# Optimization experiments

Measured on AMD Instinct MI355X. Metric: run time of the kernel, lower is better.

The kernel has to match this reference:

```python
import jax, jax.numpy as jnp
import numpy as np
from jax import lax

B, N, D, H = 8, 2048, 512, 1024


def setup_inputs() -> dict:
    key = jax.random.key(0)
    k0, k1, k2 = jax.random.split(key, 3)
    x = jax.random.normal(k0, (B, N, D), jnp.float32)
    conv_w = jax.random.normal(k1, (H, D, 3), jnp.float32) * (1.0 / np.sqrt(3 * D))
    conv_b = jnp.zeros((H,), jnp.float32)
    ln_g = jnp.ones((H,), jnp.float32)
    ln_b = jnp.zeros((H,), jnp.float32)
    proj_w = jax.random.normal(k2, (H, 2), jnp.float32) * (1.0 / np.sqrt(H))
    proj_b = jnp.zeros((2,), jnp.float32)
    return dict(x=x, conv_w=conv_w, conv_b=conv_b, ln_g=ln_g, ln_b=ln_b,
                proj_w=proj_w, proj_b=proj_b)


def reference(x, conv_w, conv_b, ln_g, ln_b, proj_w, proj_b):
    b, n, _ = x.shape
    # Conv1d(input_dim->hidden, k=3, pad=1) on [B, C, N]
    h = lax.conv_general_dilated(x.transpose(0, 2, 1), conv_w, (1,), [(1, 1)],
                                 dimension_numbers=('NCH', 'OIH', 'NCH'))
    h = h.transpose(0, 2, 1) + conv_b          # [B, N, H]
    h = jax.nn.relu(h)
    # LayerNorm over hidden dim (dropout is identity at inference)
    mu = jnp.mean(h, axis=-1, keepdims=True)
    var = jnp.mean((h - mu) ** 2, axis=-1, keepdims=True)
    h = (h - mu) * lax.rsqrt(var + 1e-5) * ln_g + ln_b
    groups_probs = h @ proj_w + proj_b          # [B, N, 2]

    g = jnp.argmax(groups_probs, axis=-1)       # [B, N] in {0,1}
    pos = jnp.arange(n)
    base = (pos + 1).astype(jnp.float32)        # 1..N
    # col 0 forced 0; start positions (g==1, pos>0) forced 0
    zero_mask = (pos[None, :] == 0) | ((g == 1) & (pos[None, :] > 0))
    vals = jnp.where(zero_mask, 0.0, jnp.broadcast_to(base[None, :], (b, n)))
    vals = vals.at[:, -1].set(float(n))         # last col = N (overrides zeroing)
    # stable descending sort by nonzero-ness == stable ascending sort by (val==0)
    order = jnp.argsort((vals == 0.0).astype(jnp.int32), axis=1)
    groups = jnp.take_along_axis(vals, order, axis=1)[:, :, None]  # [B, N, 1]

    t = base[None, None, :]                     # [1, 1, N], values 1..N
    # row 0: 1[t <= groups[:,0]]
    row0 = jnp.clip(groups[:, 0, :][:, None, :] - t + 1.0, 0.0, 1.0)      # [B, 1, N]
    # rows 1..: 1[groups[:,i-1] < t <= groups[:,i]]
    rest = (jnp.clip(groups[:, 1:, :] - t + 1.0, 0.0, 1.0)
            * jnp.clip(t - groups[:, :-1, :], 0.0, 1.0))                   # [B, N-1, N]
    grouping_matrix = jnp.concatenate([row0, rest], axis=1)                # [B, N, N]
    return (groups_probs, grouping_matrix)
```

## Files before the change

### kernel.cpp

```cpp
#include <hip/hip_runtime.h>

#define Bsz 8
#define Nsz 2048
#define Dsz 512
#define Hsz 1024
#define K3D 1536

typedef __attribute__((ext_vector_type(8))) short short8;
typedef __attribute__((ext_vector_type(4))) float f32x4;

static __device__ __forceinline__ unsigned short f2bf(float f) {
    unsigned u = __builtin_bit_cast(unsigned, f);
    unsigned r = (u + 0x7FFFu + ((u >> 16) & 1u)) >> 16;
    return (unsigned short)r;
}
static __device__ __forceinline__ float bf2f(unsigned short u) {
    return __builtin_bit_cast(float, (unsigned)u << 16);
}
static __device__ __forceinline__ void gld16(const void* g, void* l) {
    __builtin_amdgcn_global_load_lds(
        (const __attribute__((address_space(1))) void*)g,
        (__attribute__((address_space(3))) void*)l, 16, 0, 0);
}


__global__ __launch_bounds__(256) void prep_kernel(
    const float* __restrict__ cw, unsigned short* __restrict__ wsh,
    unsigned short* __restrict__ wsl,
    const float* __restrict__ lng, const float* __restrict__ lnb,
    const float* __restrict__ pw, float* __restrict__ CD,
    float* __restrict__ gq0, float* __restrict__ gq1)
{
    __shared__ float red[4][4];
    int blk = blockIdx.x, tid = threadIdx.x;
    if (blk < 192) {
        int gid = blk * 256 + tid;
        int s = gid >> 10, h = gid & 1023;
        int t = s >> 4, c = s & 15;
        const float* src = cw + (size_t)h * K3D + (size_t)c * 96 + t;
        short hv[32], lv[32];
        #pragma unroll
        for (int j = 0; j < 32; ++j) {
            float v = src[3 * j];
            unsigned short hi = f2bf(v);
            hv[j] = (short)hi;
            lv[j] = (short)f2bf(v - bf2f(hi));
        }
        #pragma unroll
        for (int m = 0; m < 4; ++m) {
            size_t dst = (((size_t)s * 4 + m) * 1024 + h) * 16;
            *(short8*)((char*)wsh + dst) = *(short8*)&hv[m * 8];
            *(short8*)((char*)wsl + dst) = *(short8*)&lv[m * 8];
        }
    } else if (blk == 192) {
        float c0 = 0.f, c1 = 0.f, d0 = 0.f, d1 = 0.f;
        for (int h = tid; h < Hsz; h += 256) {
            float g = lng[h], b = lnb[h];
            float w0 = pw[2 * h], w1 = pw[2 * h + 1];
            c0 = fmaf(g, w0, c0); c1 = fmaf(g, w1, c1);
            d0 = fmaf(b, w0, d0); d1 = fmaf(b, w1, d1);
        }
        #pragma unroll
        for (int m = 32; m >= 1; m >>= 1) {
            c0 += __shfl_xor(c0, m, 64); c1 += __shfl_xor(c1, m, 64);
            d0 += __shfl_xor(d0, m, 64); d1 += __shfl_xor(d1, m, 64);
        }
        int w = tid >> 6;
        if ((tid & 63) == 0) { red[w][0] = c0; red[w][1] = c1; red[w][2] = d0; red[w][3] = d1; }
        __syncthreads();
        if (tid == 0) {
            CD[0] = red[0][0] + red[1][0] + red[2][0] + red[3][0];
            CD[1] = red[0][1] + red[1][1] + red[2][1] + red[3][1];
            CD[2] = red[0][2] + red[1][2] + red[2][2] + red[3][2];
            CD[3] = red[0][3] + red[1][3] + red[2][3] + red[3][3];
        }
    } else {
        int h = (blk - 193) * 256 + tid;
        float g = lng[h];
        gq0[h] = g * pw[2 * h];
        gq1[h] = g * pw[2 * h + 1];
    }
}

__global__ __launch_bounds__(256) void convert_x_kernel(
    const float* __restrict__ x, unsigned short* __restrict__ xsh,
    unsigned short* __restrict__ xsl)
{
    int tid = threadIdx.x;
    int r = blockIdx.x * 4 + (tid >> 6);
    int e = tid & 63;
    int b  = r / 2050;
    int rp = r - b * 2050;
    int c  = e >> 2;
    int qq = e & 3;
    size_t dst = ((((size_t)b * 16 + c) * 4 + qq) * 2050 + rp) * 16;
    short8 hv, lv;
    if (rp == 0 || rp == 2049) {
        #pragma unroll
        for (int u = 0; u < 8; ++u) { hv[u] = 0; lv[u] = 0; }
    } else {
        const float* p = x + ((size_t)b * Nsz + (rp - 1)) * Dsz + e * 8;
        float4 v0 = *(const float4*)p;
        float4 v1 = *(const float4*)(p + 4);
        float vv[8] = { v0.x, v0.y, v0.z, v0.w, v1.x, v1.y, v1.z, v1.w };
        #pragma unroll
        for (int u = 0; u < 8; ++u) {
            unsigned short h = f2bf(vv[u]);
            hv[u] = (short)h;
            lv[u] = (short)f2bf(vv[u] - bf2f(h));
        }
    }
    *(short8*)((char*)xsh + dst) = hv;
    *(short8*)((char*)xsl + dst) = lv;
}

__global__ __launch_bounds__(512, 2) void gemm7_kernel(
    const unsigned short* __restrict__ xsh, const unsigned short* __restrict__ xsl,
    const unsigned short* __restrict__ wsh, const unsigned short* __restrict__ wsl,
    const float* __restrict__ cb, const float* __restrict__ gq0,
    const float* __restrict__ gq1, float* __restrict__ part)
{
    __shared__ __align__(16) char lds[131072];

    int tid = threadIdx.x;
    int swz = (blockIdx.x & 7) * 32 + (blockIdx.x >> 3);
    int mt  = swz >> 2;
    int ntb = swz & 3;
    int bb  = mt >> 3;
    int n0  = (mt & 7) * 256;
    int n0c = ntb * 256;
    int n0g = bb * Nsz + (mt & 7) * 256;

    int l = tid & 63, w = tid >> 6;
    int wr = w >> 2, wc = w & 3;
    int r = l & 15, qq = l >> 4;
    int aoff_r = qq * 4096 + (wr * 128 + r) * 16;
    int boff_r = qq * 4096 + (wc * 64 + r) * 16;

    const char* pAh = (const char*)xsh + (size_t)bb * 2099200 + (w & 3) * 32800 + (size_t)(n0 + l) * 16;
    const char* pAl = (const char*)xsl + (size_t)bb * 2099200 + (w & 3) * 32800 + (size_t)(n0 + l) * 16;
    const char* pBh = (const char*)wsh + (w & 3) * 16384 + (size_t)(n0c + l) * 16;
    const char* pBl = (const char*)wsl + (w & 3) * 16384 + (size_t)(n0c + l) * 16;

    f32x4 acc[8][4];
    #pragma unroll
    for (int i = 0; i < 8; ++i)
        #pragma unroll
        for (int j = 0; j < 4; ++j) acc[i][j] = (f32x4){0.f, 0.f, 0.f, 0.f};

#define STAGE(lb, sn) do {                                                     \
    if (w < 4) {                                                               \
        size_t ao = (size_t)(((sn) & 15) * 131200 + ((sn) >> 4) * 16);         \
        _Pragma("unroll") for (int g = 0; g < 4; ++g) {                        \
            gld16(pAh + ao + g * 1024, (lb) +         w * 4096 + g * 1024);    \
            gld16(pAl + ao + g * 1024, (lb) + 16384 + w * 4096 + g * 1024);    \
        }                                                                      \
    } else {                                                                   \
        size_t bo = (size_t)(sn) * 65536;                                      \
        _Pragma("unroll") for (int g = 0; g < 4; ++g) {                        \
            gld16(pBh + bo + g * 1024, (lb) + 32768 + (w - 4) * 4096 + g * 1024); \
            gld16(pBl + bo + g * 1024, (lb) + 49152 + (w - 4) * 4096 + g * 1024); \
        }                                                                      \
    }                                                                          \
} while (0)

    STAGE(lds, 0);

    for (int s = 0; s < 48; ++s) {
        char* cur = lds + (s & 1) * 65536;
        if (s < 47) {
            STAGE(lds + ((s + 1) & 1) * 65536, s + 1);
            asm volatile("s_waitcnt vmcnt(8)" ::: "memory");
        } else {
            asm volatile("s_waitcnt vmcnt(0)" ::: "memory");
        }
        __builtin_amdgcn_s_barrier();
        asm volatile("" ::: "memory");

        short8 bh[4], bl[4];
        #pragma unroll
        for (int j = 0; j < 4; ++j) {
            bh[j] = *(const short8*)(cur + 32768 + boff_r + j * 256);
            bl[j] = *(const short8*)(cur + 49152 + boff_r + j * 256);
        }
        #pragma unroll
        for (int mh = 0; mh < 2; ++mh) {
            short8 ah[4], al[4];
            #pragma unroll
            for (int i = 0; i < 4; ++i) {
                ah[i] = *(const short8*)(cur +         aoff_r + (mh * 4 + i) * 256);
                al[i] = *(const short8*)(cur + 16384 + aoff_r + (mh * 4 + i) * 256);
            }
            __builtin_amdgcn_s_setprio(1);
            #pragma unroll
            for (int i = 0; i < 4; ++i)
                #pragma unroll
                for (int j = 0; j < 4; ++j) {
                    acc[mh*4+i][j] = __builtin_amdgcn_mfma_f32_16x16x32_bf16(ah[i], bh[j], acc[mh*4+i][j], 0, 0, 0);
                    acc[mh*4+i][j] = __builtin_amdgcn_mfma_f32_16x16x32_bf16(ah[i], bl[j], acc[mh*4+i][j], 0, 0, 0);
                    acc[mh*4+i][j] = __builtin_amdgcn_mfma_f32_16x16x32_bf16(al[i], bh[j], acc[mh*4+i][j], 0, 0, 0);
                }
            __builtin_amdgcn_s_setprio(0);
        }
        __builtin_amdgcn_s_barrier();
    }
#undef STAGE

    float cbv[4], g0v[4], g1v[4];
    #pragma unroll
    for (int j = 0; j < 4; ++j) {
        int col = n0c + wc * 64 + j * 16 + r;
        cbv[j] = cb[col]; g0v[j] = gq0[col]; g1v[j] = gq1[col];
    }
    int slot = ntb * 16 + wc * 4;
    #pragma unroll
    for (int m = 0; m < 8; ++m) {
        #pragma unroll
        for (int reg = 0; reg < 4; ++reg) {
            float v0 = 0.f, v2 = 0.f, va = 0.f, vb = 0.f;
            #pragma unroll
            for (int j = 0; j < 4; ++j) {
                float v = acc[m][j][reg] + cbv[j];
                v = fmaxf(v, 0.f);
                v0 += v;
                v2 = fmaf(v, v, v2);
                va = fmaf(v, g0v[j], va);
                vb = fmaf(v, g1v[j], vb);
            }
            #pragma unroll
            for (int msk = 1; msk < 16; msk <<= 1) {
                v0 += __shfl_xor(v0, msk, 64); v2 += __shfl_xor(v2, msk, 64);
                va += __shfl_xor(va, msk, 64); vb += __shfl_xor(vb, msk, 64);
            }
            if (r == 0) {
                int rowg = n0g + wr * 128 + m * 16 + qq * 4 + reg;
                *(f32x4*)(part + (size_t)rowg * 64 + slot) = (f32x4){v0, v2, va, vb};
            }
        }
    }
}

__global__ __launch_bounds__(256) void probs_kernel(
    const float* __restrict__ part, const float* __restrict__ CD,
    const float* __restrict__ pb, float* __restrict__ probs,
    int* __restrict__ gout)
{
    int row = blockIdx.x * 256 + threadIdx.x;
    float S0 = 0.f, S2 = 0.f, Sa = 0.f, Sb = 0.f;
    const float4* p = (const float4*)(part + (size_t)row * 64);
    #pragma unroll
    for (int c = 0; c < 16; ++c) {
        float4 v = p[c];
        S0 += v.x; S2 += v.y; Sa += v.z; Sb += v.w;
    }
    float mu  = S0 * (1.0f / Hsz);
    float var = S2 * (1.0f / Hsz) - mu * mu;
    float rsq = 1.0f / sqrtf(var + 1e-5f);
    float p0 = fmaf(rsq, Sa - mu * CD[0], CD[2] + pb[0]);
    float p1 = fmaf(rsq, Sb - mu * CD[1], CD[3] + pb[1]);
    probs[(size_t)row * 2]     = p0;
    probs[(size_t)row * 2 + 1] = p1;
    gout[row] = (p1 > p0) ? 1 : 0;
}

#define ROWS 64
#define CCH 128
#define NCC (Hsz / CCH)
#define DSTEP 32

__global__ __launch_bounds__(256) void consts_kernel(
    const float* __restrict__ lng, const float* __restrict__ lnb,
    const float* __restrict__ pw, float* __restrict__ CD)
{
    int tid = threadIdx.x;
    float c0 = 0.f, c1 = 0.f, d0 = 0.f, d1 = 0.f;
    for (int h = tid; h < Hsz; h += 256) {
        float g = lng[h], b = lnb[h];
        float w0 = pw[2 * h], w1 = pw[2 * h + 1];
        c0 = fmaf(g, w0, c0); c1 = fmaf(g, w1, c1);
        d0 = fmaf(b, w0, d0); d1 = fmaf(b, w1, d1);
    }
    #pragma unroll
    for (int m = 32; m >= 1; m >>= 1) {
        c0 += __shfl_xor(c0, m, 64); c1 += __shfl_xor(c1, m, 64);
        d0 += __shfl_xor(d0, m, 64); d1 += __shfl_xor(d1, m, 64);
    }
    __shared__ float red[4][4];
    int w = tid >> 6;
    if ((tid & 63) == 0) { red[w][0] = c0; red[w][1] = c1; red[w][2] = d0; red[w][3] = d1; }
    __syncthreads();
    if (tid == 0) {
        CD[0] = red[0][0] + red[1][0] + red[2][0] + red[3][0];
        CD[1] = red[0][1] + red[1][1] + red[2][1] + red[3][1];
        CD[2] = red[0][2] + red[1][2] + red[2][2] + red[3][2];
        CD[3] = red[0][3] + red[1][3] + red[2][3] + red[3][3];
    }
}

__global__ __launch_bounds__(256) void conv_ln_proj_kernel(
    const float* __restrict__ x, const float* __restrict__ cw,
    const float* __restrict__ cb, const float* __restrict__ lng,
    const float* __restrict__ pw, const float* __restrict__ pb,
    const float* __restrict__ CD, float* __restrict__ probs,
    int* __restrict__ gout)
{
    __shared__ float Xl[DSTEP][66];
    __shared__ float Bl[3][DSTEP][CCH];
    __shared__ float Sl[ROWS][4];

    int tid = threadIdx.x;
    int blk = blockIdx.x;
    int b  = blk >> 5;
    int n0 = (blk & 31) * ROWS;
    int rg = tid >> 5;
    int cg = tid & 31;
    int sr = tid >> 2;
    int sq = tid & 3;
    const float* xb = x + (size_t)b * Nsz * Dsz;

    float s0[8], s2[8], sa[8], sb[8];
    #pragma unroll
    for (int i = 0; i < 8; ++i) { s0[i] = 0.f; s2[i] = 0.f; sa[i] = 0.f; sb[i] = 0.f; }

    for (int cc = 0; cc < NCC; ++cc) {
        float cbv[4], gq0[4], gq1[4];
        {
            int hb = cc * CCH + cg * 4;
            #pragma unroll
            for (int j = 0; j < 4; ++j) {
                int h = hb + j;
                cbv[j] = cb[h];
                float gg = lng[h];
                gq0[j] = gg * pw[2 * h];
                gq1[j] = gg * pw[2 * h + 1];
            }
        }
        float acc[8][4];
        #pragma unroll
        for (int i = 0; i < 8; ++i)
            #pragma unroll
            for (int j = 0; j < 4; ++j) acc[i][j] = 0.f;

        for (int ds = 0; ds < Dsz / DSTEP; ++ds) {
            int d0 = ds * DSTEP;
            __syncthreads();
            {
                int n = n0 - 1 + sr;
                float4 v0 = make_float4(0.f, 0.f, 0.f, 0.f), v1 = v0;
                if ((unsigned)n < (unsigned)Nsz) {
                    const float* p = xb + (size_t)n * Dsz + d0 + sq * 8;
                    v0 = *(const float4*)p;
                    v1 = *(const float4*)(p + 4);
                }
                int dd = sq * 8;
                Xl[dd + 0][sr] = v0.x; Xl[dd + 1][sr] = v0.y;
                Xl[dd + 2][sr] = v0.z; Xl[dd + 3][sr] = v0.w;
                Xl[dd + 4][sr] = v1.x; Xl[dd + 5][sr] = v1.y;
                Xl[dd + 6][sr] = v1.z; Xl[dd + 7][sr] = v1.w;
                if (tid < 8) {
                    int r2 = 64 + (tid >> 2);
                    int q2 = tid & 3;
                    int n2 = n0 - 1 + r2;
                    float4 u0 = make_float4(0.f, 0.f, 0.f, 0.f), u1 = u0;
                    if ((unsigned)n2 < (unsigned)Nsz) {
                        const float* p2 = xb + (size_t)n2 * Dsz + d0 + q2 * 8;
                        u0 = *(const float4*)p2;
                        u1 = *(const float4*)(p2 + 4);
                    }
                    int dd2 = q2 * 8;
                    Xl[dd2 + 0][r2] = u0.x; Xl[dd2 + 1][r2] = u0.y;
                    Xl[dd2 + 2][r2] = u0.z; Xl[dd2 + 3][r2] = u0.w;
                    Xl[dd2 + 4][r2] = u1.x; Xl[dd2 + 5][r2] = u1.y;
                    Xl[dd2 + 6][r2] = u1.z; Xl[dd2 + 7][r2] = u1.w;
                }
            }
            {
                int hl = tid >> 1;
                int half = tid & 1;
                const float* p = cw + (size_t)(cc * CCH + hl) * K3D + (size_t)d0 * 3 + half * 48;
                #pragma unroll
                for (int mq = 0; mq < 12; ++mq) {
                    float4 v = *(const float4*)(p + mq * 4);
                    float vv[4] = { v.x, v.y, v.z, v.w };
                    #pragma unroll
                    for (int e = 0; e < 4; ++e) {
                        int c  = mq * 4 + e;
                        int dl = half * 16 + c / 3;
                        int kk = c % 3;
                        Bl[kk][dl][hl] = vv[e];
                    }
                }
            }
            __syncthreads();
            #pragma unroll 4
            for (int dd = 0; dd < DSTEP; ++dd) {
                float a[10];
                #pragma unroll
                for (int j = 0; j < 10; ++j) a[j] = Xl[dd][rg * 8 + j];
                #pragma unroll
                for (int kk = 0; kk < 3; ++kk) {
                    float4 bv = *(const float4*)&Bl[kk][dd][cg * 4];
                    #pragma unroll
                    for (int i = 0; i < 8; ++i) {
                        float av = a[i + kk];
                        acc[i][0] = fmaf(av, bv.x, acc[i][0]);
                        acc[i][1] = fmaf(av, bv.y, acc[i][1]);
                        acc[i][2] = fmaf(av, bv.z, acc[i][2]);
                        acc[i][3] = fmaf(av, bv.w, acc[i][3]);
                    }
                }
            }
        }
        #pragma unroll
        for (int i = 0; i < 8; ++i) {
            #pragma unroll
            for (int j = 0; j < 4; ++j) {
                float v = acc[i][j] + cbv[j];
                v = fmaxf(v, 0.f);
                s0[i] += v;
                s2[i] = fmaf(v, v, s2[i]);
                sa[i] = fmaf(v, gq0[j], sa[i]);
                sb[i] = fmaf(v, gq1[j], sb[i]);
            }
        }
    }
    #pragma unroll
    for (int i = 0; i < 8; ++i) {
        float v0 = s0[i], v2 = s2[i], va = sa[i], vb = sb[i];
        #pragma unroll
        for (int mm = 16; mm >= 1; mm >>= 1) {
            v0 += __shfl_xor(v0, mm, 64); v2 += __shfl_xor(v2, mm, 64);
            va += __shfl_xor(va, mm, 64); vb += __shfl_xor(vb, mm, 64);
        }
        if (cg == 0) {
            int rr = rg * 8 + i;
            Sl[rr][0] = v0; Sl[rr][1] = v2; Sl[rr][2] = va; Sl[rr][3] = vb;
        }
    }
    __syncthreads();
    if (tid < ROWS) {
        int rr = tid, n = n0 + rr;
        float S0 = Sl[rr][0], S2 = Sl[rr][1], Sa = Sl[rr][2], Sb = Sl[rr][3];
        float mu  = S0 * (1.0f / Hsz);
        float var = S2 * (1.0f / Hsz) - mu * mu;
        float rsq = 1.0f / sqrtf(var + 1e-5f);
        float p0 = fmaf(rsq, Sa - mu * CD[0], CD[2] + pb[0]);
        float p1 = fmaf(rsq, Sb - mu * CD[1], CD[3] + pb[1]);
        size_t ro = (size_t)(b * Nsz + n);
        probs[ro * 2]     = p0;
        probs[ro * 2 + 1] = p1;
        gout[ro] = (p1 > p0) ? 1 : 0;
    }
}

__global__ __launch_bounds__(256) void bounds_kernel(
    const int* __restrict__ g, float* __restrict__ vlist, int* __restrict__ Kb)
{
    int b = blockIdx.x, tid = threadIdx.x;
    int base = tid * 8;
    int f[8]; float val[8]; int lsum = 0;
    #pragma unroll
    for (int u = 0; u < 8; ++u) {
        int i = base + u;
        int nz;
        if (i == Nsz - 1) nz = 1;
        else if (i == 0)  nz = 0;
        else              nz = (g[b * Nsz + i] == 0) ? 1 : 0;
        f[u] = nz;
        val[u] = (i == Nsz - 1) ? (float)Nsz : (float)(i + 1);
        lsum += nz;
    }
    int lane = tid & 63, w = tid >> 6;
    int sc = lsum;
    #pragma unroll
    for (int off = 1; off < 64; off <<= 1) {
        int t = __shfl_up(sc, off, 64);
        if (lane >= off) sc += t;
    }
    __shared__ int wsum[4];
    if (lane == 63) wsum[w] = sc;
    __syncthreads();
    int woff = 0;
    #pragma unroll
    for (int k = 0; k < 4; ++k) if (k < w) woff += wsum[k];
    int pos = woff + (sc - lsum);
    #pragma unroll
    for (int u = 0; u < 8; ++u) {
        if (f[u]) { vlist[b * Nsz + pos] = val[u]; pos++; }
    }
    if (tid == 255) Kb[b] = woff + sc;
}

__global__ __launch_bounds__(256) void fill_kernel(
    const float* __restrict__ vlist, const int* __restrict__ Kb,
    float* __restrict__ mat)
{
    int blk = blockIdx.x;
    int b = blk >> 11, j = blk & 2047;
    int K = Kb[b];
    float c = (j < K) ? vlist[b * Nsz + j] : 0.0f;
    float a = (j == 0) ? 0.0f : vlist[b * Nsz + j - 1];
    int tc = threadIdx.x * 8;
    float o[8];
    #pragma unroll
    for (int e = 0; e < 8; ++e) {
        float t = (float)(tc + e + 1);
        o[e] = (t > a && t <= c) ? 1.0f : 0.0f;
    }
    float4* p = (float4*)(mat + (size_t)blk * Nsz + tc);
    p[0] = make_float4(o[0], o[1], o[2], o[3]);
    p[1] = make_float4(o[4], o[5], o[6], o[7]);
}

extern "C" void kernel_launch(void* const* d_in, const int* in_sizes, int n_in,
                              void* d_out, int out_size, void* d_ws, size_t ws_size,
                              hipStream_t stream)
{
    const float* x      = (const float*)d_in[0];
    const float* conv_w = (const float*)d_in[1];
    const float* conv_b = (const float*)d_in[2];
    const float* ln_g   = (const float*)d_in[3];
    const float* ln_b   = (const float*)d_in[4];
    const float* proj_w = (const float*)d_in[5];
    const float* proj_b = (const float*)d_in[6];

    float* out = (float*)d_out;
    char*  wsb = (char*)d_ws;

    size_t cur = 0;
    auto take = [&](size_t b) { size_t r = cur; cur = (cur + b + 255) & ~(size_t)255; return r; };
    size_t oCD  = take(16);
    size_t oGQ0 = take(Hsz * 4);
    size_t oGQ1 = take(Hsz * 4);
    size_t oKb  = take(32);
    size_t oG   = take((size_t)Bsz * Nsz * 4);
    size_t oV   = take((size_t)Bsz * Nsz * 4);
    size_t oPart= take((size_t)Bsz * Nsz * 64 * 4);
    size_t oXh  = take((size_t)Bsz * 16 * 4 * 2050 * 16);
    size_t oXl  = take((size_t)Bsz * 16 * 4 * 2050 * 16);
    size_t oWh  = take((size_t)48 * 4 * 1024 * 16);
    size_t oWl  = take((size_t)48 * 4 * 1024 * 16);
    bool fast = ws_size >= cur;

    if (fast) {
        float* CD    = (float*)(wsb + oCD);
        float* gq0   = (float*)(wsb + oGQ0);
        float* gq1   = (float*)(wsb + oGQ1);
        int*   Kb    = (int*)  (wsb + oKb);
        int*   g     = (int*)  (wsb + oG);
        float* vlist = (float*)(wsb + oV);
        float* part  = (float*)(wsb + oPart);
        unsigned short* xsh = (unsigned short*)(wsb + oXh);
        unsigned short* xsl = (unsigned short*)(wsb + oXl);
        unsigned short* wsh = (unsigned short*)(wsb + oWh);
        unsigned short* wsl = (unsigned short*)(wsb + oWl);

        prep_kernel<<<197, 256, 0, stream>>>(conv_w, wsh, wsl, ln_g, ln_b, proj_w, CD, gq0, gq1);
        convert_x_kernel<<<Bsz * 2050 / 4, 256, 0, stream>>>(x, xsh, xsl);
        gemm7_kernel<<<256, 512, 0, stream>>>(
            xsh, xsl, wsh, wsl, conv_b, gq0, gq1, part);
        probs_kernel<<<Bsz * Nsz / 256, 256, 0, stream>>>(part, CD, proj_b, out, g);
        bounds_kernel<<<Bsz, 256, 0, stream>>>(g, vlist, Kb);
        fill_kernel<<<Bsz * Nsz, 256, 0, stream>>>(vlist, Kb, out + (size_t)Bsz * Nsz * 2);
    } else {
        float* wf  = (float*)d_ws;
        int*   wi  = (int*)d_ws;
        float* CD    = wf;
        int*   Kb    = wi + 4;
        int*   g     = wi + 16;
        float* vlist = wf + 16 + Bsz * Nsz;

        consts_kernel<<<1, 256, 0, stream>>>(ln_g, ln_b, proj_w, CD);
        conv_ln_proj_kernel<<<Bsz * Nsz / ROWS, 256, 0, stream>>>(
            x, conv_w, conv_b, ln_g, proj_w, proj_b, CD, out, g);
        bounds_kernel<<<Bsz, 256, 0, stream>>>(g, vlist, Kb);
        fill_kernel<<<Bsz * Nsz, 256, 0, stream>>>(vlist, Kb, out + (size_t)Bsz * Nsz * 2);
    }
}
```

Measured before the change: 182.9 us.

## Split GEMM k-step into six phases interleaving LDS reads, prefetch and MFMA

```diff
diff --git a/kernel.cpp b/kernel.cpp
--- a/kernel.cpp
+++ b/kernel.cpp
@@ -114,7 +114,7 @@
     *(short8*)((char*)xsl + dst) = lv;
 }
 
-__global__ __launch_bounds__(512, 2) void gemm7_kernel(
+__global__ __launch_bounds__(512, 2) void gemm8_kernel(
     const unsigned short* __restrict__ xsh, const unsigned short* __restrict__ xsl,
     const unsigned short* __restrict__ wsh, const unsigned short* __restrict__ wsl,
     const float* __restrict__ cb, const float* __restrict__ gq0,
@@ -148,63 +148,88 @@
         #pragma unroll
         for (int j = 0; j < 4; ++j) acc[i][j] = (f32x4){0.f, 0.f, 0.f, 0.f};
 
-#define STAGE(lb, sn) do {                                                     \
+#define STAGE2(lb, sn, pp) do {                                                \
     if (w < 4) {                                                               \
         size_t ao = (size_t)(((sn) & 15) * 131200 + ((sn) >> 4) * 16);         \
-        _Pragma("unroll") for (int g = 0; g < 4; ++g) {                        \
-            gld16(pAh + ao + g * 1024, (lb) +         w * 4096 + g * 1024);    \
-            gld16(pAl + ao + g * 1024, (lb) + 16384 + w * 4096 + g * 1024);    \
-        }                                                                      \
+        gld16(pAh + ao + (pp) * 1024, (lb) +         w * 4096 + (pp) * 1024);  \
+        gld16(pAl + ao + (pp) * 1024, (lb) + 16384 + w * 4096 + (pp) * 1024);  \
     } else {                                                                   \
         size_t bo = (size_t)(sn) * 65536;                                      \
-        _Pragma("unroll") for (int g = 0; g < 4; ++g) {                        \
-            gld16(pBh + bo + g * 1024, (lb) + 32768 + (w - 4) * 4096 + g * 1024); \
-            gld16(pBl + bo + g * 1024, (lb) + 49152 + (w - 4) * 4096 + g * 1024); \
-        }                                                                      \
+        gld16(pBh + bo + (pp) * 1024, (lb) + 32768 + (w - 4) * 4096 + (pp) * 1024); \
+        gld16(pBl + bo + (pp) * 1024, (lb) + 49152 + (w - 4) * 4096 + (pp) * 1024); \
     }                                                                          \
 } while (0)
 
-    STAGE(lds, 0);
+#define PH_SYNC() do {                                                         \
+    __builtin_amdgcn_s_barrier();                                              \
+    asm volatile("s_waitcnt lgkmcnt(0)" ::: "memory");                         \
+    __builtin_amdgcn_sched_barrier(0);                                         \
+} while (0)
+
+#define MFMA16(base, A, B) do {                                                \
+    __builtin_amdgcn_s_setprio(1);                                             \
+    _Pragma("unroll") for (int i = 0; i < 4; ++i)                              \
+        _Pragma("unroll") for (int j = 0; j < 4; ++j)                          \
+            acc[(base)+i][j] = __builtin_amdgcn_mfma_f32_16x16x32_bf16(        \
+                (A)[i], (B)[j], acc[(base)+i][j], 0, 0, 0);                    \
+    __builtin_amdgcn_s_setprio(0);                                             \
+} while (0)
+
+    STAGE2(lds, 0, 0); STAGE2(lds, 0, 1); STAGE2(lds, 0, 2); STAGE2(lds, 0, 3);
+    asm volatile("s_waitcnt vmcnt(0)" ::: "memory");
+    __builtin_amdgcn_s_barrier();
 
     for (int s = 0; s < 48; ++s) {
         char* cur = lds + (s & 1) * 65536;
-        if (s < 47) {
-            STAGE(lds + ((s + 1) & 1) * 65536, s + 1);
-            asm volatile("s_waitcnt vmcnt(8)" ::: "memory");
-        } else {
-            asm volatile("s_waitcnt vmcnt(0)" ::: "memory");
-        }
+        char* nxt = lds + ((s + 1) & 1) * 65536;
+        bool pf = (s < 47);
+        int sn = s + 1;
+        short8 ah[4], al[4], bh[4], bl[4];
+
+        #pragma unroll
+        for (int j = 0; j < 4; ++j) bh[j] = *(const short8*)(cur + 32768 + boff_r + j * 256);
+        #pragma unroll
+        for (int i = 0; i < 4; ++i) ah[i] = *(const short8*)(cur + aoff_r + i * 256);
+        if (pf) STAGE2(nxt, sn, 0);
+        PH_SYNC();
+        MFMA16(0, ah, bh);
         __builtin_amdgcn_s_barrier();
-        asm volatile("" ::: "memory");
-
-        short8 bh[4], bl[4];
-        #pragma unroll
-        for (int j = 0; j < 4; ++j) {
-            bh[j] = *(const short8*)(cur + 32768 + boff_r + j * 256);
-            bl[j] = *(const short8*)(cur + 49152 + boff_r + j * 256);
-        }
-        #pragma unroll
-        for (int mh = 0; mh < 2; ++mh) {
-            short8 ah[4], al[4];
-            #pragma unroll
-            for (int i = 0; i < 4; ++i) {
-                ah[i] = *(const short8*)(cur +         aoff_r + (mh * 4 + i) * 256);
-                al[i] = *(const short8*)(cur + 16384 + aoff_r + (mh * 4 + i) * 256);
-            }
-            __builtin_amdgcn_s_setprio(1);
-            #pragma unroll
-            for (int i = 0; i < 4; ++i)
-                #pragma unroll
-                for (int j = 0; j < 4; ++j) {
-                    acc[mh*4+i][j] = __builtin_amdgcn_mfma_f32_16x16x32_bf16(ah[i], bh[j], acc[mh*4+i][j], 0, 0, 0);
-                    acc[mh*4+i][j] = __builtin_amdgcn_mfma_f32_16x16x32_bf16(ah[i], bl[j], acc[mh*4+i][j], 0, 0, 0);
-                    acc[mh*4+i][j] = __builtin_amdgcn_mfma_f32_16x16x32_bf16(al[i], bh[j], acc[mh*4+i][j], 0, 0, 0);
-                }
-            __builtin_amdgcn_s_setprio(0);
-        }
+
+        #pragma unroll
+        for (int i = 0; i < 4; ++i) al[i] = *(const short8*)(cur + 16384 + aoff_r + i * 256);
+        if (pf) STAGE2(nxt, sn, 1);
+        PH_SYNC();
+        MFMA16(0, al, bh);
         __builtin_amdgcn_s_barrier();
-    }
-#undef STAGE
+
+        #pragma unroll
+        for (int j = 0; j < 4; ++j) bl[j] = *(const short8*)(cur + 49152 + boff_r + j * 256);
+        if (pf) STAGE2(nxt, sn, 2);
+        PH_SYNC();
+        MFMA16(0, ah, bl);
+        __builtin_amdgcn_s_barrier();
+
+        #pragma unroll
+        for (int i = 0; i < 4; ++i) ah[i] = *(const short8*)(cur + aoff_r + (4 + i) * 256);
+        if (pf) STAGE2(nxt, sn, 3);
+        PH_SYNC();
+        MFMA16(4, ah, bh);
+        __builtin_amdgcn_s_barrier();
+
+        #pragma unroll
+        for (int i = 0; i < 4; ++i) al[i] = *(const short8*)(cur + 16384 + aoff_r + (4 + i) * 256);
+        PH_SYNC();
+        MFMA16(4, al, bh);
+        __builtin_amdgcn_s_barrier();
+
+        PH_SYNC();
+        MFMA16(4, ah, bl);
+        asm volatile("s_waitcnt vmcnt(0)" ::: "memory");
+        __builtin_amdgcn_s_barrier();
+    }
+#undef STAGE2
+#undef PH_SYNC
+#undef MFMA16
 
     float cbv[4], g0v[4], g1v[4];
     #pragma unroll
@@ -557,7 +582,7 @@
 
         prep_kernel<<<197, 256, 0, stream>>>(conv_w, wsh, wsl, ln_g, ln_b, proj_w, CD, gq0, gq1);
         convert_x_kernel<<<Bsz * 2050 / 4, 256, 0, stream>>>(x, xsh, xsl);
-        gemm7_kernel<<<256, 512, 0, stream>>>(
+        gemm8_kernel<<<256, 512, 0, stream>>>(
             xsh, xsl, wsh, wsl, conv_b, gq0, gq1, part);
         probs_kernel<<<Bsz * Nsz / 256, 256, 0, stream>>>(part, CD, proj_b, out, g);
         bounds_kernel<<<Bsz, 256, 0, stream>>>(g, vlist, Kb);
```

Result: no change. 186.1 us (+1.7%).

## Load B operands directly to registers and halve LDS staging in GEMM

Applied to the files above, without the earlier changes.

```diff
diff --git a/kernel.cpp b/kernel.cpp
--- a/kernel.cpp
+++ b/kernel.cpp
@@ -114,18 +114,19 @@
     *(short8*)((char*)xsl + dst) = lv;
 }
 
-__global__ __launch_bounds__(512, 2) void gemm7_kernel(
+__global__ __launch_bounds__(512, 2) void gemm9_kernel(
     const unsigned short* __restrict__ xsh, const unsigned short* __restrict__ xsl,
     const unsigned short* __restrict__ wsh, const unsigned short* __restrict__ wsl,
     const float* __restrict__ cb, const float* __restrict__ gq0,
     const float* __restrict__ gq1, float* __restrict__ part)
 {
-    __shared__ __align__(16) char lds[131072];
+    __shared__ __align__(16) char lds[65536];
 
     int tid = threadIdx.x;
-    int swz = (blockIdx.x & 7) * 32 + (blockIdx.x >> 3);
-    int mt  = swz >> 2;
-    int ntb = swz & 3;
+    int bid = blockIdx.x;
+    int xcd = bid & 7, idx = bid >> 3;
+    int mt  = (xcd >> 1) * 16 + (idx >> 1);
+    int ntb = (xcd & 1) * 2 + (idx & 1);
     int bb  = mt >> 3;
     int n0  = (mt & 7) * 256;
     int n0c = ntb * 256;
@@ -135,12 +136,13 @@
     int wr = w >> 2, wc = w & 3;
     int r = l & 15, qq = l >> 4;
     int aoff_r = qq * 4096 + (wr * 128 + r) * 16;
-    int boff_r = qq * 4096 + (wc * 64 + r) * 16;
-
-    const char* pAh = (const char*)xsh + (size_t)bb * 2099200 + (w & 3) * 32800 + (size_t)(n0 + l) * 16;
-    const char* pAl = (const char*)xsl + (size_t)bb * 2099200 + (w & 3) * 32800 + (size_t)(n0 + l) * 16;
-    const char* pBh = (const char*)wsh + (w & 3) * 16384 + (size_t)(n0c + l) * 16;
-    const char* pBl = (const char*)wsl + (w & 3) * 16384 + (size_t)(n0c + l) * 16;
+
+    const char* pA = (const char*)(w < 4 ? xsh : xsl)
+                   + (size_t)bb * 2099200 + (w & 3) * 32800 + (size_t)(n0 + l) * 16;
+    int ldsAw = ((w & 4) ? 16384 : 0) + (w & 3) * 4096;
+
+    const char* pBh = (const char*)wsh + qq * 16384 + (size_t)(n0c + wc * 64 + r) * 16;
+    const char* pBl = (const char*)wsl + qq * 16384 + (size_t)(n0c + wc * 64 + r) * 16;
 
     f32x4 acc[8][4];
     #pragma unroll
@@ -148,63 +150,58 @@
         #pragma unroll
         for (int j = 0; j < 4; ++j) acc[i][j] = (f32x4){0.f, 0.f, 0.f, 0.f};
 
-#define STAGE(lb, sn) do {                                                     \
-    if (w < 4) {                                                               \
-        size_t ao = (size_t)(((sn) & 15) * 131200 + ((sn) >> 4) * 16);         \
-        _Pragma("unroll") for (int g = 0; g < 4; ++g) {                        \
-            gld16(pAh + ao + g * 1024, (lb) +         w * 4096 + g * 1024);    \
-            gld16(pAl + ao + g * 1024, (lb) + 16384 + w * 4096 + g * 1024);    \
-        }                                                                      \
-    } else {                                                                   \
-        size_t bo = (size_t)(sn) * 65536;                                      \
-        _Pragma("unroll") for (int g = 0; g < 4; ++g) {                        \
-            gld16(pBh + bo + g * 1024, (lb) + 32768 + (w - 4) * 4096 + g * 1024); \
-            gld16(pBl + bo + g * 1024, (lb) + 49152 + (w - 4) * 4096 + g * 1024); \
-        }                                                                      \
-    }                                                                          \
-} while (0)
-
-    STAGE(lds, 0);
-
-    for (int s = 0; s < 48; ++s) {
-        char* cur = lds + (s & 1) * 65536;
-        if (s < 47) {
-            STAGE(lds + ((s + 1) & 1) * 65536, s + 1);
-            asm volatile("s_waitcnt vmcnt(8)" ::: "memory");
+    short8 bh0[4], bl0[4], bh1[4], bl1[4];
+
+#define LOADB(BH, BL, sn) do { size_t o = (size_t)(sn) * 65536;                \
+    _Pragma("unroll") for (int j = 0; j < 4; ++j) {                            \
+        BH[j] = *(const short8*)(pBh + o + j * 256);                           \
+        BL[j] = *(const short8*)(pBl + o + j * 256); } } while (0)
+
+#define STAGEA(lb, sn) do {                                                    \
+    size_t ao = (size_t)(((sn) & 15) * 131200 + ((sn) >> 4) * 16);             \
+    _Pragma("unroll") for (int g = 0; g < 4; ++g)                              \
+        gld16(pA + ao + g * 1024, (lb) + ldsAw + g * 1024); } while (0)
+
+#define COMPUTE(buf, BH, BL) do {                                              \
+    _Pragma("unroll") for (int mh = 0; mh < 2; ++mh) {                         \
+        short8 ah[4], al[4];                                                   \
+        _Pragma("unroll") for (int i = 0; i < 4; ++i) {                        \
+            ah[i] = *(const short8*)((buf) + aoff_r + (mh * 4 + i) * 256);     \
+            al[i] = *(const short8*)((buf) + 16384 + aoff_r + (mh * 4 + i) * 256); } \
+        __builtin_amdgcn_s_setprio(1);                                         \
+        _Pragma("unroll") for (int i = 0; i < 4; ++i)                          \
+            _Pragma("unroll") for (int j = 0; j < 4; ++j) {                    \
+                acc[mh*4+i][j] = __builtin_amdgcn_mfma_f32_16x16x32_bf16(ah[i], BH[j], acc[mh*4+i][j], 0, 0, 0); \
+                acc[mh*4+i][j] = __builtin_amdgcn_mfma_f32_16x16x32_bf16(ah[i], BL[j], acc[mh*4+i][j], 0, 0, 0); \
+                acc[mh*4+i][j] = __builtin_amdgcn_mfma_f32_16x16x32_bf16(al[i], BH[j], acc[mh*4+i][j], 0, 0, 0); } \
+        __builtin_amdgcn_s_setprio(0);                                         \
+    } } while (0)
+
+    LOADB(bh0, bl0, 0);
+    STAGEA(lds, 0);
+
+    for (int sp = 0; sp < 24; ++sp) {
+        int s0 = sp * 2, s1 = s0 + 1;
+        LOADB(bh1, bl1, s1);
+        STAGEA(lds + 32768, s1);
+        asm volatile("s_waitcnt vmcnt(12)" ::: "memory");
+        __builtin_amdgcn_s_barrier();
+        COMPUTE(lds, bh0, bl0);
+        __builtin_amdgcn_s_barrier();
+        if (s1 < 47) {
+            LOADB(bh0, bl0, s1 + 1);
+            STAGEA(lds, s1 + 1);
+            asm volatile("s_waitcnt vmcnt(12)" ::: "memory");
         } else {
             asm volatile("s_waitcnt vmcnt(0)" ::: "memory");
         }
         __builtin_amdgcn_s_barrier();
-        asm volatile("" ::: "memory");
-
-        short8 bh[4], bl[4];
-        #pragma unroll
-        for (int j = 0; j < 4; ++j) {
-            bh[j] = *(const short8*)(cur + 32768 + boff_r + j * 256);
-            bl[j] = *(const short8*)(cur + 49152 + boff_r + j * 256);
-        }
-        #pragma unroll
-        for (int mh = 0; mh < 2; ++mh) {
-            short8 ah[4], al[4];
-            #pragma unroll
-            for (int i = 0; i < 4; ++i) {
-                ah[i] = *(const short8*)(cur +         aoff_r + (mh * 4 + i) * 256);
-                al[i] = *(const short8*)(cur + 16384 + aoff_r + (mh * 4 + i) * 256);
-            }
-            __builtin_amdgcn_s_setprio(1);
-            #pragma unroll
-            for (int i = 0; i < 4; ++i)
-                #pragma unroll
-                for (int j = 0; j < 4; ++j) {
-                    acc[mh*4+i][j] = __builtin_amdgcn_mfma_f32_16x16x32_bf16(ah[i], bh[j], acc[mh*4+i][j], 0, 0, 0);
-                    acc[mh*4+i][j] = __builtin_amdgcn_mfma_f32_16x16x32_bf16(ah[i], bl[j], acc[mh*4+i][j], 0, 0, 0);
-                    acc[mh*4+i][j] = __builtin_amdgcn_mfma_f32_16x16x32_bf16(al[i], bh[j], acc[mh*4+i][j], 0, 0, 0);
-                }
-            __builtin_amdgcn_s_setprio(0);
-        }
+        COMPUTE(lds + 32768, bh1, bl1);
         __builtin_amdgcn_s_barrier();
     }
-#undef STAGE
+#undef LOADB
+#undef STAGEA
+#undef COMPUTE
 
     float cbv[4], g0v[4], g1v[4];
     #pragma unroll
@@ -557,7 +554,7 @@
 
         prep_kernel<<<197, 256, 0, stream>>>(conv_w, wsh, wsl, ln_g, ln_b, proj_w, CD, gq0, gq1);
         convert_x_kernel<<<Bsz * 2050 / 4, 256, 0, stream>>>(x, xsh, xsl);
-        gemm7_kernel<<<256, 512, 0, stream>>>(
+        gemm9_kernel<<<256, 512, 0, stream>>>(
             xsh, xsl, wsh, wsl, conv_b, gq0, gq1, part);
         probs_kernel<<<Bsz * Nsz / 256, 256, 0, stream>>>(part, CD, proj_b, out, g);
         bounds_kernel<<<Bsz, 256, 0, stream>>>(g, vlist, Kb);
```

Result: slower. 187.8 us (+2.6%).
